# Optimization experiments

Measured on AMD Instinct MI355X. Metric: run time of the kernel, lower is better.

The kernel has to match this reference:

```python
import jax, jax.numpy as jnp
import numpy as np

T, D, H = 32768, 64, 128  # timesteps, input_size, hidden_size

def setup_inputs() -> dict:
    key = jax.random.key(0)
    ks = jax.random.split(key, 13)
    s_ih = 1.0 / np.sqrt(H)
    def u(k, shape):
        return jax.random.uniform(k, shape, jnp.float32, -s_ih, s_ih)
    return {
        "X": jax.random.normal(ks[0], (T, 1, D), jnp.float32),
        "W_ih": u(ks[1], (4 * H, D)),
        "W_hh": u(ks[2], (4 * H, H)),
        "b_ih": u(ks[3], (4 * H,)),
        "b_hh": u(ks[4], (4 * H,)),
        "W1": u(ks[5], (11, H)), "b1": u(ks[6], (11,)),
        "W2": u(ks[7], (2, H)),  "b2": u(ks[8], (2,)),
        "W3": u(ks[9], (1, H)),  "b3": u(ks[10], (1,)),
        "W4": u(ks[11], (1, H)), "b4": u(ks[12], (1,)),
    }

def reference(X, W_ih, W_hh, b_ih, b_hh, W1, b1, W2, b2, W3, b3, W4, b4):
    # LSTMCell recurrence over T steps, batch=1 (masks are identity: Dropout(p=0) on ones)
    def cell(carry, x):
        h, c = carry  # [1,H]
        gates = x @ W_ih.T + b_ih + h @ W_hh.T + b_hh  # [1,4H]
        i, f, g, o = jnp.split(gates, 4, axis=-1)
        c2 = jax.nn.sigmoid(f) * c + jax.nn.sigmoid(i) * jnp.tanh(g)
        h2 = jax.nn.sigmoid(o) * jnp.tanh(c2)
        return (h2, c2), h2

    h0 = jnp.zeros((1, H), X.dtype)
    c0 = jnp.zeros((1, H), X.dtype)
    _, hs = jax.lax.scan(cell, (h0, c0), X)  # hs: [T,1,H]
    out = hs[:, 0, :]  # squeeze -> [T,H]

    # MtFc head: 4 small linears on the same features
    step = out @ W1.T + b1        # [T,11]
    experience = out @ W2.T + b2  # [T,2]
    rsd = out @ W3.T + b3         # [T,1]
    s = out @ W4.T + b4           # [T,1]
    return (step, experience, rsd, s)
```

## Files before the change

### kernel.cpp

```cpp
#include <hip/hip_runtime.h>
#include <hip/hip_bf16.h>
#include <cstdint>
#include <cstddef>

#define T_STEPS 32768
#define DD 64
#define HH 128
#define GG 512

#define OFF_EXP 360448
#define OFF_RSD 425984
#define OFF_S   458752

typedef __attribute__((ext_vector_type(8))) _Float16 half8;
typedef __attribute__((ext_vector_type(4))) float f32x4;

__device__ __forceinline__ float exp2_f(float x) {
    float r; asm("v_exp_f32 %0, %1" : "=v"(r) : "v"(x)); return r;
}

__device__ __forceinline__ int grow_of(int j) {
    return (j & 3) * HH + (j >> 6) * 16 + ((j >> 4) & 3) * 4 + ((j & 15) >> 2);
}

__global__ __launch_bounds__(512, 2) void pregate_kernel(
    const float* __restrict__ X, const float* __restrict__ W_ih,
    const float* __restrict__ b_ih, const float* __restrict__ b_hh,
    float* __restrict__ P, int t0, int nrows)
{
    __shared__ __align__(16) float xs[DD];
    const int j = threadIdx.x;
    const int grow = grow_of(j);

    float w[DD];
    const float4* wv = reinterpret_cast<const float4*>(W_ih + (size_t)grow * DD);
#pragma unroll
    for (int k = 0; k < DD / 4; ++k) {
        float4 v = wv[k];
        w[4*k+0] = v.x; w[4*k+1] = v.y; w[4*k+2] = v.z; w[4*k+3] = v.w;
    }
    const float bias = b_ih[grow] + b_hh[grow];

    const int rpb = (nrows + gridDim.x - 1) / gridDim.x;
    const int r0  = blockIdx.x * rpb;
    const int r1  = (r0 + rpb < nrows) ? (r0 + rpb) : nrows;

    for (int r = r0; r < r1; ++r) {
        const int t = t0 + r;
        if (j < DD) xs[j] = X[(size_t)t * DD + j];
        __syncthreads();
        float acc = bias;
        const float4* xv = reinterpret_cast<const float4*>(xs);
#pragma unroll
        for (int k = 0; k < DD / 4; ++k) {
            float4 v = xv[k];
            acc += v.x*w[4*k+0] + v.y*w[4*k+1] + v.z*w[4*k+2] + v.w*w[4*k+3];
        }
        P[(size_t)r * GG + j] = acc;
        __syncthreads();
    }
}

__global__ __launch_bounds__(512, 2) void lstm_seq_kernel(
    const float* __restrict__ P, const float* __restrict__ W_hh,
    float* __restrict__ hist, float* __restrict__ state,
    int t0, int C)
{
    __shared__ __align__(16) _Float16 hh2[2][HH];
    __shared__ __align__(16) float gate_lds[GG];

    const int j    = threadIdx.x;
    const int w    = j >> 6;
    const int l    = j & 63;
    const int col  = l & 15;
    const int kgrp = l >> 4;
    const int gt   = l & 3;

    half8 wf[4][4];
#pragma unroll
    for (int mt = 0; mt < 4; ++mt) {
        const int growB = gt * HH + 16 * w + 4 * mt + (col >> 2);
        const float* wr = W_hh + (size_t)growB * HH + 8 * kgrp;
#pragma unroll
        for (int kt = 0; kt < 4; ++kt) {
            const float* wp = wr + 32 * kt;
            float4 w0 = *reinterpret_cast<const float4*>(wp);
            float4 w1 = *reinterpret_cast<const float4*>(wp + 4);
            half8 hf;
            hf[0] = (_Float16)w0.x; hf[1] = (_Float16)w0.y;
            hf[2] = (_Float16)w0.z; hf[3] = (_Float16)w0.w;
            hf[4] = (_Float16)w1.x; hf[5] = (_Float16)w1.y;
            hf[6] = (_Float16)w1.z; hf[7] = (_Float16)w1.w;
            wf[mt][kt] = hf;
        }
    }

    const bool  isg = (gt == 2);
    const float sA  = isg ?  2.885390082f : -1.442695041f;
    const float sB  = isg ? -2.0f : 1.0f;
    const float sC  = isg ?  1.0f : 0.0f;
    const bool  b0  = (kgrp & 1) != 0;
    const bool  b1  = (kgrp & 2) != 0;

    const int mycell = 16 * w + l;
    float c = 0.0f;
    if (t0 != 0 && l < 16) c = state[HH + mycell];
    if (j < HH) hh2[0][j] = (_Float16)((t0 != 0) ? state[j] : 0.0f);
    __syncthreads();

    float pcq = P[j];
    float pn1 = (C > 1) ? P[GG + j] : 0.0f;
    const float* pp = P + 2 * (size_t)GG + j;
    float* hw = hist + mycell;
    float hn = 0.0f;
    const f32x4 Z = {0.0f, 0.0f, 0.0f, 0.0f};

#pragma unroll 1
    for (int r = 0; r < C; ++r) {
        const _Float16* hb = &hh2[r & 1][8 * kgrp];
        const half8 a0 = *reinterpret_cast<const half8*>(hb);
        const half8 a1 = *reinterpret_cast<const half8*>(hb + 32);
        const half8 a2 = *reinterpret_cast<const half8*>(hb + 64);
        const half8 a3 = *reinterpret_cast<const half8*>(hb + 96);

        float pn2 = 0.0f;
        if (r + 2 < C) pn2 = *pp;
        pp += GG;

        f32x4 q0 = __builtin_amdgcn_mfma_f32_16x16x32_f16(a0, wf[0][0], Z, 0, 0, 0);
        f32x4 q1 = __builtin_amdgcn_mfma_f32_16x16x32_f16(a0, wf[1][0], Z, 0, 0, 0);
        f32x4 q2 = __builtin_amdgcn_mfma_f32_16x16x32_f16(a0, wf[2][0], Z, 0, 0, 0);
        f32x4 q3 = __builtin_amdgcn_mfma_f32_16x16x32_f16(a0, wf[3][0], Z, 0, 0, 0);
        q0 = __builtin_amdgcn_mfma_f32_16x16x32_f16(a1, wf[0][1], q0, 0, 0, 0);
        q1 = __builtin_amdgcn_mfma_f32_16x16x32_f16(a1, wf[1][1], q1, 0, 0, 0);
        q2 = __builtin_amdgcn_mfma_f32_16x16x32_f16(a1, wf[2][1], q2, 0, 0, 0);
        q3 = __builtin_amdgcn_mfma_f32_16x16x32_f16(a1, wf[3][1], q3, 0, 0, 0);
        q0 = __builtin_amdgcn_mfma_f32_16x16x32_f16(a2, wf[0][2], q0, 0, 0, 0);
        q1 = __builtin_amdgcn_mfma_f32_16x16x32_f16(a2, wf[1][2], q1, 0, 0, 0);
        q2 = __builtin_amdgcn_mfma_f32_16x16x32_f16(a2, wf[2][2], q2, 0, 0, 0);
        q3 = __builtin_amdgcn_mfma_f32_16x16x32_f16(a2, wf[3][2], q3, 0, 0, 0);
        q0 = __builtin_amdgcn_mfma_f32_16x16x32_f16(a3, wf[0][3], q0, 0, 0, 0);
        q1 = __builtin_amdgcn_mfma_f32_16x16x32_f16(a3, wf[1][3], q1, 0, 0, 0);
        q2 = __builtin_amdgcn_mfma_f32_16x16x32_f16(a3, wf[2][3], q2, 0, 0, 0);
        q3 = __builtin_amdgcn_mfma_f32_16x16x32_f16(a3, wf[3][3], q3, 0, 0, 0);

        const float s01  = b0 ? q1[0] : q0[0];
        const float s23  = b0 ? q3[0] : q2[0];
        const float ssum = b1 ? s23 : s01;

        const float pre = ssum + pcq;
        const float t   = __builtin_amdgcn_rcpf(1.0f + exp2_f(pre * sA));
        const float a   = __builtin_fmaf(t, sB, sC);

        gate_lds[64 * w + 16 * kgrp + col] = a;
        asm volatile("s_waitcnt lgkmcnt(0)" ::: "memory");

        if (l < 16) {
            const f32x4 g4 = *reinterpret_cast<const f32x4*>(&gate_lds[64 * w + 4 * l]);
            c = __builtin_fmaf(g4[1], c, g4[0] * g4[2]);
            const float tc = __builtin_amdgcn_rcpf(1.0f + exp2_f(c * 2.885390082f));
            hn = g4[3] * __builtin_fmaf(tc, -2.0f, 1.0f);
            hh2[(r & 1) ^ 1][mycell] = (_Float16)hn;
            *hw = hn;
        }
        hw += HH;
        pcq = pn1; pn1 = pn2;

        asm volatile("s_waitcnt lgkmcnt(0)" ::: "memory");
        __builtin_amdgcn_s_barrier();
        __builtin_amdgcn_sched_barrier(0);
    }

    if (l < 16) {
        state[mycell]      = hn;
        state[HH + mycell] = c;
    }
}

__global__ __launch_bounds__(256, 4) void heads_kernel(
    const float* __restrict__ hist,
    const float* __restrict__ W1, const float* __restrict__ b1,
    const float* __restrict__ W2, const float* __restrict__ b2,
    const float* __restrict__ W3, const float* __restrict__ b3,
    const float* __restrict__ W4, const float* __restrict__ b4,
    float* __restrict__ out, int t0, int C)
{
    const int idx = blockIdx.x * 256 + threadIdx.x;
    const int tr  = idx >> 4;
    const int oi  = idx & 15;
    if (tr >= C || oi >= 15) return;

    const float* wrow;
    float bias;
    if (oi < 11)       { wrow = W1 + oi * HH;        bias = b1[oi]; }
    else if (oi < 13)  { wrow = W2 + (oi - 11) * HH; bias = b2[oi - 11]; }
    else if (oi == 13) { wrow = W3;                  bias = b3[0]; }
    else               { wrow = W4;                  bias = b4[0]; }

    const float4* h4 = reinterpret_cast<const float4*>(hist + (size_t)tr * HH);
    const float4* w4 = reinterpret_cast<const float4*>(wrow);
    float s = bias;
#pragma unroll
    for (int k = 0; k < HH / 4; ++k) {
        float4 hv = h4[k];
        float4 wv = w4[k];
        s += hv.x*wv.x + hv.y*wv.y + hv.z*wv.z + hv.w*wv.w;
    }
    const int t = t0 + tr;
    if (oi < 11)       out[(size_t)t * 11 + oi] = s;
    else if (oi < 13)  out[OFF_EXP + (size_t)t * 2 + (oi - 11)] = s;
    else if (oi == 13) out[OFF_RSD + t] = s;
    else               out[OFF_S + t] = s;
}

extern "C" void kernel_launch(void* const* d_in, const int* in_sizes, int n_in,
                              void* d_out, int out_size, void* d_ws, size_t ws_size,
                              hipStream_t stream)
{
    const float* X    = (const float*)d_in[0];
    const float* W_ih = (const float*)d_in[1];
    const float* W_hh = (const float*)d_in[2];
    const float* b_ih = (const float*)d_in[3];
    const float* b_hh = (const float*)d_in[4];
    const float* W1   = (const float*)d_in[5];
    const float* b1   = (const float*)d_in[6];
    const float* W2   = (const float*)d_in[7];
    const float* b2   = (const float*)d_in[8];
    const float* W3   = (const float*)d_in[9];
    const float* b3   = (const float*)d_in[10];
    const float* W4   = (const float*)d_in[11];
    const float* b4   = (const float*)d_in[12];

    float* out   = (float*)d_out;
    float* state = (float*)d_ws;

    size_t avail = (ws_size > 1024) ? (ws_size - 1024) / 2560 : 0;
    int C = (avail >= (size_t)T_STEPS) ? T_STEPS : (int)avail;
    if (C < 1) C = 1;
    float* hist = state + 256;
    float* P    = hist + (size_t)C * HH;

    for (int t0 = 0; t0 < T_STEPS; t0 += C) {
        const int Cc = (C < T_STEPS - t0) ? C : (T_STEPS - t0);
        const int nb = (Cc < 512) ? Cc : 512;
        pregate_kernel<<<nb, 512, 0, stream>>>(X, W_ih, b_ih, b_hh, P, t0, Cc);
        lstm_seq_kernel<<<1, 512, 0, stream>>>(P, W_hh, hist, state, t0, Cc);
        heads_kernel<<<(Cc * 16 + 255) / 256, 256, 0, stream>>>(
            hist, W1, b1, W2, b2, W3, b3, W4, b4, out, t0, Cc);
    }
}
```

Baseline: 16.58 ms.

## Compute all four gates per lane and drop LDS gate exchange in LSTM step

```diff
diff --git a/kernel.cpp b/kernel.cpp
--- a/kernel.cpp
+++ b/kernel.cpp
@@ -18,9 +18,12 @@
 __device__ __forceinline__ float exp2_f(float x) {
     float r; asm("v_exp_f32 %0, %1" : "=v"(r) : "v"(x)); return r;
 }
-
-__device__ __forceinline__ int grow_of(int j) {
-    return (j & 3) * HH + (j >> 6) * 16 + ((j >> 4) & 3) * 4 + ((j & 15) >> 2);
+__device__ __forceinline__ float sigm_fast(float x) {
+    return __builtin_amdgcn_rcpf(1.0f + exp2_f(x * -1.442695041f));
+}
+__device__ __forceinline__ float tanh_fast(float x) {
+    return __builtin_fmaf(
+        __builtin_amdgcn_rcpf(1.0f + exp2_f(x * 2.885390082f)), -2.0f, 1.0f);
 }
 
 __global__ __launch_bounds__(512, 2) void pregate_kernel(
@@ -30,7 +33,7 @@
 {
     __shared__ __align__(16) float xs[DD];
     const int j = threadIdx.x;
-    const int grow = grow_of(j);
+    const int grow = (j & 3) * HH + (j >> 2);
 
     float w[DD];
     const float4* wv = reinterpret_cast<const float4*>(W_ih + (size_t)grow * DD);
@@ -67,20 +70,18 @@
     int t0, int C)
 {
     __shared__ __align__(16) _Float16 hh2[2][HH];
-    __shared__ __align__(16) float gate_lds[GG];
-
-    const int j    = threadIdx.x;
-    const int w    = j >> 6;
-    const int l    = j & 63;
-    const int col  = l & 15;
-    const int kgrp = l >> 4;
-    const int gt   = l & 3;
+
+    const int j      = threadIdx.x;
+    const int w      = j >> 6;
+    const int l      = j & 63;
+    const int col    = l & 15;
+    const int kgrp   = l >> 4;
+    const int mycell = 16 * w + col;
 
     half8 wf[4][4];
 #pragma unroll
     for (int mt = 0; mt < 4; ++mt) {
-        const int growB = gt * HH + 16 * w + 4 * mt + (col >> 2);
-        const float* wr = W_hh + (size_t)growB * HH + 8 * kgrp;
+        const float* wr = W_hh + (size_t)(mt * HH + mycell) * HH + 8 * kgrp;
 #pragma unroll
         for (int kt = 0; kt < 4; ++kt) {
             const float* wp = wr + 32 * kt;
@@ -95,25 +96,16 @@
         }
     }
 
-    const bool  isg = (gt == 2);
-    const float sA  = isg ?  2.885390082f : -1.442695041f;
-    const float sB  = isg ? -2.0f : 1.0f;
-    const float sC  = isg ?  1.0f : 0.0f;
-    const bool  b0  = (kgrp & 1) != 0;
-    const bool  b1  = (kgrp & 2) != 0;
-
-    const int mycell = 16 * w + l;
     float c = 0.0f;
-    if (t0 != 0 && l < 16) c = state[HH + mycell];
+    if (t0 != 0) c = state[HH + mycell];
     if (j < HH) hh2[0][j] = (_Float16)((t0 != 0) ? state[j] : 0.0f);
     __syncthreads();
 
-    float pcq = P[j];
-    float pn1 = (C > 1) ? P[GG + j] : 0.0f;
-    const float* pp = P + 2 * (size_t)GG + j;
-    float* hw = hist + mycell;
+    const float* Pme = P + 4 * (size_t)mycell;
+    const f32x4 Z = {0.0f, 0.0f, 0.0f, 0.0f};
+    f32x4 pc  = *reinterpret_cast<const f32x4*>(Pme);
+    f32x4 pn1 = (C > 1) ? *reinterpret_cast<const f32x4*>(Pme + GG) : Z;
     float hn = 0.0f;
-    const f32x4 Z = {0.0f, 0.0f, 0.0f, 0.0f};
 
 #pragma unroll 1
     for (int r = 0; r < C; ++r) {
@@ -123,55 +115,42 @@
         const half8 a2 = *reinterpret_cast<const half8*>(hb + 64);
         const half8 a3 = *reinterpret_cast<const half8*>(hb + 96);
 
-        float pn2 = 0.0f;
-        if (r + 2 < C) pn2 = *pp;
-        pp += GG;
-
-        f32x4 q0 = __builtin_amdgcn_mfma_f32_16x16x32_f16(a0, wf[0][0], Z, 0, 0, 0);
-        f32x4 q1 = __builtin_amdgcn_mfma_f32_16x16x32_f16(a0, wf[1][0], Z, 0, 0, 0);
-        f32x4 q2 = __builtin_amdgcn_mfma_f32_16x16x32_f16(a0, wf[2][0], Z, 0, 0, 0);
-        f32x4 q3 = __builtin_amdgcn_mfma_f32_16x16x32_f16(a0, wf[3][0], Z, 0, 0, 0);
-        q0 = __builtin_amdgcn_mfma_f32_16x16x32_f16(a1, wf[0][1], q0, 0, 0, 0);
-        q1 = __builtin_amdgcn_mfma_f32_16x16x32_f16(a1, wf[1][1], q1, 0, 0, 0);
-        q2 = __builtin_amdgcn_mfma_f32_16x16x32_f16(a1, wf[2][1], q2, 0, 0, 0);
-        q3 = __builtin_amdgcn_mfma_f32_16x16x32_f16(a1, wf[3][1], q3, 0, 0, 0);
-        q0 = __builtin_amdgcn_mfma_f32_16x16x32_f16(a2, wf[0][2], q0, 0, 0, 0);
-        q1 = __builtin_amdgcn_mfma_f32_16x16x32_f16(a2, wf[1][2], q1, 0, 0, 0);
-        q2 = __builtin_amdgcn_mfma_f32_16x16x32_f16(a2, wf[2][2], q2, 0, 0, 0);
-        q3 = __builtin_amdgcn_mfma_f32_16x16x32_f16(a2, wf[3][2], q3, 0, 0, 0);
-        q0 = __builtin_amdgcn_mfma_f32_16x16x32_f16(a3, wf[0][3], q0, 0, 0, 0);
-        q1 = __builtin_amdgcn_mfma_f32_16x16x32_f16(a3, wf[1][3], q1, 0, 0, 0);
-        q2 = __builtin_amdgcn_mfma_f32_16x16x32_f16(a3, wf[2][3], q2, 0, 0, 0);
-        q3 = __builtin_amdgcn_mfma_f32_16x16x32_f16(a3, wf[3][3], q3, 0, 0, 0);
-
-        const float s01  = b0 ? q1[0] : q0[0];
-        const float s23  = b0 ? q3[0] : q2[0];
-        const float ssum = b1 ? s23 : s01;
-
-        const float pre = ssum + pcq;
-        const float t   = __builtin_amdgcn_rcpf(1.0f + exp2_f(pre * sA));
-        const float a   = __builtin_fmaf(t, sB, sC);
-
-        gate_lds[64 * w + 16 * kgrp + col] = a;
-        asm volatile("s_waitcnt lgkmcnt(0)" ::: "memory");
-
-        if (l < 16) {
-            const f32x4 g4 = *reinterpret_cast<const f32x4*>(&gate_lds[64 * w + 4 * l]);
-            c = __builtin_fmaf(g4[1], c, g4[0] * g4[2]);
-            const float tc = __builtin_amdgcn_rcpf(1.0f + exp2_f(c * 2.885390082f));
-            hn = g4[3] * __builtin_fmaf(tc, -2.0f, 1.0f);
-            hh2[(r & 1) ^ 1][mycell] = (_Float16)hn;
-            *hw = hn;
-        }
-        hw += HH;
-        pcq = pn1; pn1 = pn2;
+        f32x4 pn2 = Z;
+        if (r + 2 < C) pn2 = *reinterpret_cast<const f32x4*>(Pme + (size_t)(r + 2) * GG);
+
+#define M(A, B) __builtin_amdgcn_mfma_f32_16x16x32_f16((A), (B), Z, 0, 0, 0)
+        f32x4 d00 = M(a0, wf[0][0]); f32x4 d01 = M(a1, wf[0][1]);
+        f32x4 d02 = M(a2, wf[0][2]); f32x4 d03 = M(a3, wf[0][3]);
+        f32x4 d10 = M(a0, wf[1][0]); f32x4 d11 = M(a1, wf[1][1]);
+        f32x4 d12 = M(a2, wf[1][2]); f32x4 d13 = M(a3, wf[1][3]);
+        f32x4 d20 = M(a0, wf[2][0]); f32x4 d21 = M(a1, wf[2][1]);
+        f32x4 d22 = M(a2, wf[2][2]); f32x4 d23 = M(a3, wf[2][3]);
+        f32x4 d30 = M(a0, wf[3][0]); f32x4 d31 = M(a1, wf[3][1]);
+        f32x4 d32 = M(a2, wf[3][2]); f32x4 d33 = M(a3, wf[3][3]);
+#undef M
+        const float si = (d00[0] + d01[0]) + (d02[0] + d03[0]);
+        const float sf = (d10[0] + d11[0]) + (d12[0] + d13[0]);
+        const float sg = (d20[0] + d21[0]) + (d22[0] + d23[0]);
+        const float so = (d30[0] + d31[0]) + (d32[0] + d33[0]);
+
+        const float ai = sigm_fast(si + pc[0]);
+        const float af = sigm_fast(sf + pc[1]);
+        const float ag = tanh_fast(sg + pc[2]);
+        const float ao = sigm_fast(so + pc[3]);
+        c = __builtin_fmaf(af, c, ai * ag);
+        hn = ao * tanh_fast(c);
+
+        if (kgrp == 0)      hh2[(r & 1) ^ 1][mycell] = (_Float16)hn;
+        else if (kgrp == 1) hist[(size_t)r * HH + mycell] = hn;
+
+        pc = pn1; pn1 = pn2;
 
         asm volatile("s_waitcnt lgkmcnt(0)" ::: "memory");
         __builtin_amdgcn_s_barrier();
         __builtin_amdgcn_sched_barrier(0);
     }
 
-    if (l < 16) {
+    if (kgrp == 0) {
         state[mycell]      = hn;
         state[HH + mycell] = c;
     }
```

After: 22.18 ms. 1.34x slower.
